# Kernel tuning notes

Measured on AMD Instinct MI355X. Metric: run time of the kernel, lower is better.

Reference implementation:

```python
import jax, jax.numpy as jnp
import numpy as np

K = 3  # number_layers

def setup_inputs() -> dict:
    key = jax.random.key(0)
    k1, k2, k3, k4 = jax.random.split(key, 4)
    N, F_in, F_out, E, D = 100000, 256, 64, 1600000, 8
    x = jax.random.normal(k1, (N, F_in), dtype=jnp.float32)
    edge_attr = jax.random.uniform(k2, (E, D), dtype=jnp.float32)
    W = jax.random.normal(k3, (F_in, F_out), dtype=jnp.float32) / np.sqrt(F_in)
    b = jnp.zeros((F_out,), dtype=jnp.float32)
    edge_index = jax.random.randint(k4, (2, E), 0, N, dtype=jnp.int64)
    return {"x": x, "edge_attr": edge_attr, "W": W, "b": b, "edge_index": edge_index}

def reference(x, edge_attr, W, b, edge_index):
    N = x.shape[0]
    # edge_weight from edge_attr
    w = edge_attr.mean(axis=1)  # [E]
    src, dst = edge_index[0], edge_index[1]
    # gcn_norm: add self-loops with weight 1, symmetric normalization
    loop = jnp.arange(N, dtype=edge_index.dtype)
    src_f = jnp.concatenate([src, loop])
    dst_f = jnp.concatenate([dst, loop])
    w_f = jnp.concatenate([w, jnp.ones((N,), dtype=x.dtype)])
    deg = jax.ops.segment_sum(w_f, dst_f, num_segments=N)  # in-degree
    dinv = jnp.where(deg > 0, jax.lax.rsqrt(deg), 0.0)
    norm = dinv[src_f] * w_f * dinv[dst_f]  # [E+N]
    # K hops of x <- A_hat x
    h = x
    for _ in range(K):
        msg = norm[:, None] * h[src_f]              # gather [E+N, F]
        h = jax.ops.segment_sum(msg, dst_f, num_segments=N)  # scatter-add
    out = h @ W + b
    out = jax.nn.relu(out)
    # dropout is a no-op in eval mode
    return jax.nn.log_softmax(out, axis=-1)
```

## Files before the change

### kernel.cpp

```cpp
#include <hip/hip_runtime.h>
#include <hip/hip_bf16.h>


#define F_IN 256
#define F_OUT 64


__global__ __launch_bounds__(256) void init_kernel(int* __restrict__ cnt, int N) {
    int i = blockIdx.x * 256 + threadIdx.x;
    if (i < N) cnt[i] = 0;
}

__global__ __launch_bounds__(256) void hist_kernel(const int* __restrict__ ei_dst,
                                                   int E, int N, int* __restrict__ cnt) {
    int e = blockIdx.x * 256 + threadIdx.x;
    if (e >= E) return;
    int d = ei_dst[e];
    if ((unsigned)d >= (unsigned)N) return;
    atomicAdd(&cnt[d], 1);
}

__global__ __launch_bounds__(256) void scan1_kernel(const int* __restrict__ cnt, int* __restrict__ ptr,
                                                    int* __restrict__ bsum, int N) {
    __shared__ int s[256];
    int tid = threadIdx.x;
    int base = blockIdx.x * 1024 + tid * 4;
    int c0 = (base + 0 < N) ? cnt[base + 0] : 0;
    int c1 = (base + 1 < N) ? cnt[base + 1] : 0;
    int c2 = (base + 2 < N) ? cnt[base + 2] : 0;
    int c3 = (base + 3 < N) ? cnt[base + 3] : 0;
    int tsum = c0 + c1 + c2 + c3;
    s[tid] = tsum;
    __syncthreads();
    for (int off = 1; off < 256; off <<= 1) {
        int t = (tid >= off) ? s[tid - off] : 0;
        __syncthreads();
        s[tid] += t;
        __syncthreads();
    }
    int excl = s[tid] - tsum;
    if (base + 0 < N) ptr[base + 0] = excl;
    if (base + 1 < N) ptr[base + 1] = excl + c0;
    if (base + 2 < N) ptr[base + 2] = excl + c0 + c1;
    if (base + 3 < N) ptr[base + 3] = excl + c0 + c1 + c2;
    if (tid == 255) bsum[blockIdx.x] = s[255];
}

__global__ __launch_bounds__(256) void scan2_kernel(const int* __restrict__ bsum, int* __restrict__ bscan, int nb) {
    __shared__ int s[256];
    int tid = threadIdx.x;
    int v = (tid < nb) ? bsum[tid] : 0;
    s[tid] = v;
    __syncthreads();
    for (int off = 1; off < 256; off <<= 1) {
        int t = (tid >= off) ? s[tid - off] : 0;
        __syncthreads();
        s[tid] += t;
        __syncthreads();
    }
    if (tid < nb) bscan[tid] = s[tid] - v;
}

__global__ __launch_bounds__(256) void scan3_kernel(int* __restrict__ ptr, const int* __restrict__ bscan,
                                                    int* __restrict__ cursor, int N) {
    int i = blockIdx.x * 256 + threadIdx.x;
    if (i < N) {
        int p = ptr[i] + bscan[i >> 10];
        ptr[i] = p;
        cursor[i] = p;
    }
}

__global__ __launch_bounds__(256) void fill_kernel(const int* __restrict__ ei,
                                                   const float* __restrict__ ea,
                                                   int* __restrict__ cursor,
                                                   int2* __restrict__ csr, int E, int N) {
    int e = blockIdx.x * 256 + threadIdx.x;
    if (e >= E) return;
    int s = ei[e];
    int d = ei[E + e];
    if ((unsigned)s >= (unsigned)N || (unsigned)d >= (unsigned)N) return;
    const float4* a = (const float4*)(ea + (size_t)e * 8);
    float4 a0 = a[0], a1 = a[1];
    float wv = (a0.x + a0.y + a0.z + a0.w + a1.x + a1.y + a1.z + a1.w) * 0.125f;
    int slot = atomicAdd(&cursor[d], 1);
    csr[slot] = make_int2(s, __float_as_int(wv));
}

__global__ __launch_bounds__(256) void degk_kernel(const int* __restrict__ ptr, const int* __restrict__ cnt,
                                                   const int2* __restrict__ csr,
                                                   float* __restrict__ dinv, int N) {
    int i = blockIdx.x * 256 + threadIdx.x;
    if (i >= N) return;
    int p = ptr[i], c = cnt[i];
    float deg = 1.0f;
    for (int j = 0; j < c; ++j) deg += __int_as_float(csr[p + j].y);
    dinv[i] = rsqrtf(deg);
}

#define ACC4(A, XV) \
    A.x = fmaf(XV.x, w0.x, A.x); A.y = fmaf(XV.x, w0.y, A.y); A.z = fmaf(XV.x, w0.z, A.z); A.w = fmaf(XV.x, w0.w, A.w); \
    A.x = fmaf(XV.y, w1.x, A.x); A.y = fmaf(XV.y, w1.y, A.y); A.z = fmaf(XV.y, w1.z, A.z); A.w = fmaf(XV.y, w1.w, A.w); \
    A.x = fmaf(XV.z, w2.x, A.x); A.y = fmaf(XV.z, w2.y, A.y); A.z = fmaf(XV.z, w2.z, A.z); A.w = fmaf(XV.z, w2.w, A.w); \
    A.x = fmaf(XV.w, w3.x, A.x); A.y = fmaf(XV.w, w3.y, A.y); A.z = fmaf(XV.w, w3.z, A.z); A.w = fmaf(XV.w, w3.w, A.w);

__global__ __launch_bounds__(1024) void xw_kernel(const float* __restrict__ x, const float* __restrict__ W,
                                                  const float* __restrict__ dinv,
                                                  float* __restrict__ y, int N) {
    __shared__ float Wl[F_IN * F_OUT];
    const float4* W4 = (const float4*)W;
    float4* Wl4 = (float4*)Wl;
    for (int i = threadIdx.x; i < F_IN * F_OUT / 4; i += 1024) Wl4[i] = W4[i];
    __syncthreads();

    int gwave = (blockIdx.x * 1024 + threadIdx.x) >> 6;
    int nwaves = (gridDim.x * 1024) >> 6;
    int lane = threadIdx.x & 63;
    int r = lane >> 4;
    int jg = lane & 15;
    int ngroups = (N + 15) >> 4;

    for (int g = gwave; g < ngroups; g += nwaves) {
        int row0 = g * 16 + r * 4;
        float4 a0 = {0,0,0,0}, a1 = {0,0,0,0}, a2 = {0,0,0,0}, a3 = {0,0,0,0};
        if (row0 + 3 < N) {
            const float4* xr0 = (const float4*)(x + (size_t)(row0 + 0) * F_IN);
            const float4* xr1 = (const float4*)(x + (size_t)(row0 + 1) * F_IN);
            const float4* xr2 = (const float4*)(x + (size_t)(row0 + 2) * F_IN);
            const float4* xr3 = (const float4*)(x + (size_t)(row0 + 3) * F_IN);
#pragma unroll 2
            for (int k4 = 0; k4 < F_IN / 4; ++k4) {
                float4 xv0 = xr0[k4];
                float4 xv1 = xr1[k4];
                float4 xv2 = xr2[k4];
                float4 xv3 = xr3[k4];
                float4 w0 = Wl4[(k4 * 4 + 0) * 16 + jg];
                float4 w1 = Wl4[(k4 * 4 + 1) * 16 + jg];
                float4 w2 = Wl4[(k4 * 4 + 2) * 16 + jg];
                float4 w3 = Wl4[(k4 * 4 + 3) * 16 + jg];
                ACC4(a0, xv0)
                ACC4(a1, xv1)
                ACC4(a2, xv2)
                ACC4(a3, xv3)
            }
            float d0 = dinv[row0 + 0], d1 = dinv[row0 + 1], d2 = dinv[row0 + 2], d3 = dinv[row0 + 3];
            a0.x *= d0; a0.y *= d0; a0.z *= d0; a0.w *= d0;
            a1.x *= d1; a1.y *= d1; a1.z *= d1; a1.w *= d1;
            a2.x *= d2; a2.y *= d2; a2.z *= d2; a2.w *= d2;
            a3.x *= d3; a3.y *= d3; a3.z *= d3; a3.w *= d3;
            ((float4*)(y + (size_t)(row0 + 0) * F_OUT))[jg] = a0;
            ((float4*)(y + (size_t)(row0 + 1) * F_OUT))[jg] = a1;
            ((float4*)(y + (size_t)(row0 + 2) * F_OUT))[jg] = a2;
            ((float4*)(y + (size_t)(row0 + 3) * F_OUT))[jg] = a3;
        } else {
            for (int i4 = 0; i4 < 4; ++i4) {
                int row = row0 + i4;
                if (row >= N) break;
                const float4* xr = (const float4*)(x + (size_t)row * F_IN);
                float4 a = {0,0,0,0};
                for (int k4 = 0; k4 < F_IN / 4; ++k4) {
                    float4 xv = xr[k4];
                    float4 w0 = Wl4[(k4 * 4 + 0) * 16 + jg];
                    float4 w1 = Wl4[(k4 * 4 + 1) * 16 + jg];
                    float4 w2 = Wl4[(k4 * 4 + 2) * 16 + jg];
                    float4 w3 = Wl4[(k4 * 4 + 3) * 16 + jg];
                    ACC4(a, xv)
                }
                float di = dinv[row];
                a.x *= di; a.y *= di; a.z *= di; a.w *= di;
                ((float4*)(y + (size_t)row * F_OUT))[jg] = a;
            }
        }
    }
}

__global__ __launch_bounds__(256) void prop_kernel(const float* __restrict__ gin, float* __restrict__ gout,
                                                   const int* __restrict__ ptr, const int* __restrict__ cnt,
                                                   const float* __restrict__ dinv,
                                                   const int2* __restrict__ csr, int N) {
    int node = blockIdx.x * 4 + (threadIdx.x >> 6);
    if (node >= N) return;
    int lane = threadIdx.x & 63;
    float acc = gin[(size_t)node * 64 + lane];
    int p = ptr[node], c = cnt[node];
    int i = 0;
    for (; i + 8 <= c; i += 8) {
        int2 e0 = csr[p + i + 0];
        int2 e1 = csr[p + i + 1];
        int2 e2 = csr[p + i + 2];
        int2 e3 = csr[p + i + 3];
        int2 e4 = csr[p + i + 4];
        int2 e5 = csr[p + i + 5];
        int2 e6 = csr[p + i + 6];
        int2 e7 = csr[p + i + 7];
        float v0 = gin[(size_t)e0.x * 64 + lane];
        float v1 = gin[(size_t)e1.x * 64 + lane];
        float v2 = gin[(size_t)e2.x * 64 + lane];
        float v3 = gin[(size_t)e3.x * 64 + lane];
        float v4 = gin[(size_t)e4.x * 64 + lane];
        float v5 = gin[(size_t)e5.x * 64 + lane];
        float v6 = gin[(size_t)e6.x * 64 + lane];
        float v7 = gin[(size_t)e7.x * 64 + lane];
        acc = fmaf(__int_as_float(e0.y), v0, acc);
        acc = fmaf(__int_as_float(e1.y), v1, acc);
        acc = fmaf(__int_as_float(e2.y), v2, acc);
        acc = fmaf(__int_as_float(e3.y), v3, acc);
        acc = fmaf(__int_as_float(e4.y), v4, acc);
        acc = fmaf(__int_as_float(e5.y), v5, acc);
        acc = fmaf(__int_as_float(e6.y), v6, acc);
        acc = fmaf(__int_as_float(e7.y), v7, acc);
    }
    for (; i < c; ++i) {
        int2 e = csr[p + i];
        acc = fmaf(__int_as_float(e.y), gin[(size_t)e.x * 64 + lane], acc);
    }
    float di = dinv[node];
    gout[(size_t)node * 64 + lane] = acc * di * di;
}

__global__ __launch_bounds__(256) void prop_final_kernel(const float* __restrict__ gin, float* __restrict__ out,
                                                         const int* __restrict__ ptr, const int* __restrict__ cnt,
                                                         const float* __restrict__ dinv,
                                                         const int2* __restrict__ csr,
                                                         const float* __restrict__ b, int N) {
    int node = blockIdx.x * 4 + (threadIdx.x >> 6);
    if (node >= N) return;
    int lane = threadIdx.x & 63;
    float acc = gin[(size_t)node * 64 + lane];
    int p = ptr[node], c = cnt[node];
    int i = 0;
    for (; i + 8 <= c; i += 8) {
        int2 e0 = csr[p + i + 0];
        int2 e1 = csr[p + i + 1];
        int2 e2 = csr[p + i + 2];
        int2 e3 = csr[p + i + 3];
        int2 e4 = csr[p + i + 4];
        int2 e5 = csr[p + i + 5];
        int2 e6 = csr[p + i + 6];
        int2 e7 = csr[p + i + 7];
        float v0 = gin[(size_t)e0.x * 64 + lane];
        float v1 = gin[(size_t)e1.x * 64 + lane];
        float v2 = gin[(size_t)e2.x * 64 + lane];
        float v3 = gin[(size_t)e3.x * 64 + lane];
        float v4 = gin[(size_t)e4.x * 64 + lane];
        float v5 = gin[(size_t)e5.x * 64 + lane];
        float v6 = gin[(size_t)e6.x * 64 + lane];
        float v7 = gin[(size_t)e7.x * 64 + lane];
        acc = fmaf(__int_as_float(e0.y), v0, acc);
        acc = fmaf(__int_as_float(e1.y), v1, acc);
        acc = fmaf(__int_as_float(e2.y), v2, acc);
        acc = fmaf(__int_as_float(e3.y), v3, acc);
        acc = fmaf(__int_as_float(e4.y), v4, acc);
        acc = fmaf(__int_as_float(e5.y), v5, acc);
        acc = fmaf(__int_as_float(e6.y), v6, acc);
        acc = fmaf(__int_as_float(e7.y), v7, acc);
    }
    for (; i < c; ++i) {
        int2 e = csr[p + i];
        acc = fmaf(__int_as_float(e.y), gin[(size_t)e.x * 64 + lane], acc);
    }
    float v = acc * dinv[node] + b[lane];
    v = fmaxf(v, 0.0f);
    float m = v;
    for (int off = 32; off; off >>= 1) m = fmaxf(m, __shfl_xor(m, off, 64));
    float ex = expf(v - m);
    float s = ex;
    for (int off = 32; off; off >>= 1) s += __shfl_xor(s, off, 64);
    out[(size_t)node * 64 + lane] = (v - m) - logf(s);
}


extern "C" void kernel_launch(void* const* d_in, const int* in_sizes, int n_in,
                              void* d_out, int out_size, void* d_ws, size_t ws_size,
                              hipStream_t stream) {
    const float* x = (const float*)d_in[0];
    const float* edge_attr = (const float*)d_in[1];
    const float* W = (const float*)d_in[2];
    const float* b = (const float*)d_in[3];
    const int* ei = (const int*)d_in[4];
    int N = in_sizes[0] / F_IN;
    int E = in_sizes[4] / 2;
    float* out = (float*)d_out;

    char* ws = (char*)d_ws;
    size_t off = 0;
    auto alloc = [&](size_t bytes) -> char* {
        char* p = ws + off;
        off += (bytes + 255) & ~(size_t)255;
        return p;
    };
    float* dinv    = (float*)alloc((size_t)N * 4);
    int*   cnt     = (int*)alloc((size_t)N * 4);
    int*   ptr     = (int*)alloc((size_t)N * 4);
    int*   cursor  = (int*)alloc((size_t)N * 4);
    int*   bsum    = (int*)alloc(256 * 4);
    int*   bscan   = (int*)alloc(256 * 4);
    int2*  csr     = (int2*)alloc((size_t)E * 8);
    float* h0      = (float*)alloc((size_t)N * 64 * 4);
    float* h1      = (float*)alloc((size_t)N * 64 * 4);

    int nbN = (N + 255) / 256;
    int nbE = (E + 255) / 256;
    int nb1024 = (N + 1023) / 1024;
    int nbNode4 = (N + 3) / 4;

    init_kernel<<<nbN, 256, 0, stream>>>(cnt, N);
    hist_kernel<<<nbE, 256, 0, stream>>>(ei + E, E, N, cnt);
    scan1_kernel<<<nb1024, 256, 0, stream>>>(cnt, ptr, bsum, N);
    scan2_kernel<<<1, 256, 0, stream>>>(bsum, bscan, nb1024);
    scan3_kernel<<<nbN, 256, 0, stream>>>(ptr, bscan, cursor, N);
    fill_kernel<<<nbE, 256, 0, stream>>>(ei, edge_attr, cursor, csr, E, N);
    degk_kernel<<<nbN, 256, 0, stream>>>(ptr, cnt, csr, dinv, N);

    xw_kernel<<<256, 1024, 0, stream>>>(x, W, dinv, h0, N);

    prop_kernel<<<nbNode4, 256, 0, stream>>>(h0, h1, ptr, cnt, dinv, csr, N);
    prop_kernel<<<nbNode4, 256, 0, stream>>>(h1, h0, ptr, cnt, dinv, csr, N);
    prop_final_kernel<<<nbNode4, 256, 0, stream>>>(h0, out, ptr, cnt, dinv, csr, b, N);
}
```

Baseline: 641.9 us.

## Record per-edge atomic rank in histogram pass to drop second atomic pass

The histogram kernel now computes the edge weight and stores each edge's atomicAdd return value as its rank within its destination bucket. The fill kernel then writes CSR entries at ptr[d]+rank with no atomics, and the cursor array is removed. The xw kernel also gets an occupancy hint in launch_bounds and twice as many blocks. The cost is two extra E-sized arrays (w, seq) written and read back, in exchange for removing one pass of contended atomics.

Result: faster. 610.6 us (-4.9%).

```diff
diff --git a/kernel.cpp b/kernel.cpp
--- a/kernel.cpp
+++ b/kernel.cpp
@@ -11,13 +11,21 @@
     if (i < N) cnt[i] = 0;
 }
 
-__global__ __launch_bounds__(256) void hist_kernel(const int* __restrict__ ei_dst,
-                                                   int E, int N, int* __restrict__ cnt) {
+__global__ __launch_bounds__(256) void pass1_kernel(const float* __restrict__ ea,
+                                                    const int* __restrict__ ei_dst,
+                                                    int E, int N,
+                                                    float* __restrict__ w,
+                                                    int* __restrict__ seq,
+                                                    int* __restrict__ cnt) {
     int e = blockIdx.x * 256 + threadIdx.x;
     if (e >= E) return;
+    const float4* a = (const float4*)(ea + (size_t)e * 8);
+    float4 a0 = a[0], a1 = a[1];
+    float wv = (a0.x + a0.y + a0.z + a0.w + a1.x + a1.y + a1.z + a1.w) * 0.125f;
+    w[e] = wv;
     int d = ei_dst[e];
-    if ((unsigned)d >= (unsigned)N) return;
-    atomicAdd(&cnt[d], 1);
+    if ((unsigned)d >= (unsigned)N) { seq[e] = -1; return; }
+    seq[e] = atomicAdd(&cnt[d], 1);
 }
 
 __global__ __launch_bounds__(256) void scan1_kernel(const int* __restrict__ cnt, int* __restrict__ ptr,
@@ -61,30 +69,23 @@
     if (tid < nb) bscan[tid] = s[tid] - v;
 }
 
-__global__ __launch_bounds__(256) void scan3_kernel(int* __restrict__ ptr, const int* __restrict__ bscan,
-                                                    int* __restrict__ cursor, int N) {
+__global__ __launch_bounds__(256) void scan3_kernel(int* __restrict__ ptr, const int* __restrict__ bscan, int N) {
     int i = blockIdx.x * 256 + threadIdx.x;
-    if (i < N) {
-        int p = ptr[i] + bscan[i >> 10];
-        ptr[i] = p;
-        cursor[i] = p;
-    }
-}
-
-__global__ __launch_bounds__(256) void fill_kernel(const int* __restrict__ ei,
-                                                   const float* __restrict__ ea,
-                                                   int* __restrict__ cursor,
-                                                   int2* __restrict__ csr, int E, int N) {
+    if (i < N) ptr[i] += bscan[i >> 10];
+}
+
+__global__ __launch_bounds__(256) void pass2_kernel(const int* __restrict__ ei,
+                                                    const float* __restrict__ w,
+                                                    const int* __restrict__ seq,
+                                                    const int* __restrict__ ptr,
+                                                    int2* __restrict__ csr, int E, int N) {
     int e = blockIdx.x * 256 + threadIdx.x;
     if (e >= E) return;
     int s = ei[e];
     int d = ei[E + e];
-    if ((unsigned)s >= (unsigned)N || (unsigned)d >= (unsigned)N) return;
-    const float4* a = (const float4*)(ea + (size_t)e * 8);
-    float4 a0 = a[0], a1 = a[1];
-    float wv = (a0.x + a0.y + a0.z + a0.w + a1.x + a1.y + a1.z + a1.w) * 0.125f;
-    int slot = atomicAdd(&cursor[d], 1);
-    csr[slot] = make_int2(s, __float_as_int(wv));
+    int q = seq[e];
+    if ((unsigned)s >= (unsigned)N || (unsigned)d >= (unsigned)N || q < 0) return;
+    csr[ptr[d] + q] = make_int2(s, __float_as_int(w[e]));
 }
 
 __global__ __launch_bounds__(256) void degk_kernel(const int* __restrict__ ptr, const int* __restrict__ cnt,
@@ -104,9 +105,9 @@
     A.x = fmaf(XV.z, w2.x, A.x); A.y = fmaf(XV.z, w2.y, A.y); A.z = fmaf(XV.z, w2.z, A.z); A.w = fmaf(XV.z, w2.w, A.w); \
     A.x = fmaf(XV.w, w3.x, A.x); A.y = fmaf(XV.w, w3.y, A.y); A.z = fmaf(XV.w, w3.z, A.z); A.w = fmaf(XV.w, w3.w, A.w);
 
-__global__ __launch_bounds__(1024) void xw_kernel(const float* __restrict__ x, const float* __restrict__ W,
-                                                  const float* __restrict__ dinv,
-                                                  float* __restrict__ y, int N) {
+__global__ __launch_bounds__(1024, 8) void xw_kernel(const float* __restrict__ x, const float* __restrict__ W,
+                                                     const float* __restrict__ dinv,
+                                                     float* __restrict__ y, int N) {
     __shared__ float Wl[F_IN * F_OUT];
     const float4* W4 = (const float4*)W;
     float4* Wl4 = (float4*)Wl;
@@ -292,9 +293,10 @@
     float* dinv    = (float*)alloc((size_t)N * 4);
     int*   cnt     = (int*)alloc((size_t)N * 4);
     int*   ptr     = (int*)alloc((size_t)N * 4);
-    int*   cursor  = (int*)alloc((size_t)N * 4);
     int*   bsum    = (int*)alloc(256 * 4);
     int*   bscan   = (int*)alloc(256 * 4);
+    float* w       = (float*)alloc((size_t)E * 4);
+    int*   seq     = (int*)alloc((size_t)E * 4);
     int2*  csr     = (int2*)alloc((size_t)E * 8);
     float* h0      = (float*)alloc((size_t)N * 64 * 4);
     float* h1      = (float*)alloc((size_t)N * 64 * 4);
@@ -305,14 +307,14 @@
     int nbNode4 = (N + 3) / 4;
 
     init_kernel<<<nbN, 256, 0, stream>>>(cnt, N);
-    hist_kernel<<<nbE, 256, 0, stream>>>(ei + E, E, N, cnt);
+    pass1_kernel<<<nbE, 256, 0, stream>>>(edge_attr, ei + E, E, N, w, seq, cnt);
     scan1_kernel<<<nb1024, 256, 0, stream>>>(cnt, ptr, bsum, N);
     scan2_kernel<<<1, 256, 0, stream>>>(bsum, bscan, nb1024);
-    scan3_kernel<<<nbN, 256, 0, stream>>>(ptr, bscan, cursor, N);
-    fill_kernel<<<nbE, 256, 0, stream>>>(ei, edge_attr, cursor, csr, E, N);
+    scan3_kernel<<<nbN, 256, 0, stream>>>(ptr, bscan, N);
+    pass2_kernel<<<nbE, 256, 0, stream>>>(ei, w, seq, ptr, csr, E, N);
     degk_kernel<<<nbN, 256, 0, stream>>>(ptr, cnt, csr, dinv, N);
 
-    xw_kernel<<<256, 1024, 0, stream>>>(x, W, dinv, h0, N);
+    xw_kernel<<<512, 1024, 0, stream>>>(x, W, dinv, h0, N);
 
     prop_kernel<<<nbNode4, 256, 0, stream>>>(h0, h1, ptr, cnt, dinv, csr, N);
     prop_kernel<<<nbNode4, 256, 0, stream>>>(h1, h0, ptr, cnt, dinv, csr, N);
```
